# Kernel tuning notes

Hardware: AMD Instinct MI355X
Metric: run time of the kernel (lower is better)

Reference implementation:

```python
import jax, jax.numpy as jnp
import numpy as np

VOCAB = 32000
EMB = 512
HID = 1024
B = 64
LPRE = 256
MAXL = 16


def _gru(x, Wih, Whh, bih, bhh):
    # x: (B, T, E); torch GRU gate order r, z, n
    Bb, T, E = x.shape
    H = Whh.shape[1]
    xW = jnp.einsum('bte,ge->btg', x, Wih) + bih  # (B, T, 3H)
    def step(h, xt):
        gh = h @ Whh.T + bhh
        r = jax.nn.sigmoid(xt[:, :H] + gh[:, :H])
        z = jax.nn.sigmoid(xt[:, H:2 * H] + gh[:, H:2 * H])
        n = jnp.tanh(xt[:, 2 * H:] + r * gh[:, 2 * H:])
        h = (1.0 - z) * n + z * h
        return h, h
    h0 = jnp.zeros((Bb, H), x.dtype)
    hT, ys = jax.lax.scan(step, h0, jnp.swapaxes(xW, 0, 1))
    return jnp.swapaxes(ys, 0, 1), hT


def setup_inputs() -> dict:
    key = jax.random.key(0)
    ks = jax.random.split(key, 24)
    s = 0.02
    inp = {
        'pre_seq': jax.random.randint(ks[0], (B, LPRE), 0, VOCAB),
        'post_seq': jax.random.randint(ks[1], (B, LPRE), 0, VOCAB),
        'trg': jax.random.randint(ks[2], (B, MAXL), 0, 2),
        'emb': jax.random.normal(ks[3], (VOCAB, EMB), jnp.float32) * s,
        'Wih_pre': jax.random.normal(ks[4], (3 * HID, EMB), jnp.float32) * s,
        'Whh_pre': jax.random.normal(ks[5], (3 * HID, HID), jnp.float32) * s,
        'bih_pre': jnp.zeros((3 * HID,), jnp.float32),
        'bhh_pre': jnp.zeros((3 * HID,), jnp.float32),
        'Wih_post': jax.random.normal(ks[6], (3 * HID, EMB), jnp.float32) * s,
        'Whh_post': jax.random.normal(ks[7], (3 * HID, HID), jnp.float32) * s,
        'bih_post': jnp.zeros((3 * HID,), jnp.float32),
        'bhh_post': jnp.zeros((3 * HID,), jnp.float32),
        'fc_W': jax.random.normal(ks[8], (HID, 2 * HID), jnp.float32) * s,
        'fc_b': jnp.zeros((HID,), jnp.float32),
        'attn_W': jax.random.normal(ks[9], (HID, 2 * HID), jnp.float32) * s,
        'attn_b': jnp.zeros((HID,), jnp.float32),
        'v_W': jax.random.normal(ks[10], (1, HID), jnp.float32) * s,
        'fc1_W': jax.random.normal(ks[11], (HID, HID), jnp.float32) * s,
        'fc1_b': jnp.zeros((HID,), jnp.float32),
        'fc2_W': jax.random.normal(ks[12], (HID, 2 * HID), jnp.float32) * s,
        'fc2_b': jnp.zeros((HID,), jnp.float32),
        'fco_W': jax.random.normal(ks[13], (1, 2 * HID), jnp.float32) * s,
        'fco_b': jnp.zeros((1,), jnp.float32),
    }
    return inp


def reference(pre_seq, post_seq, trg, emb,
              Wih_pre, Whh_pre, bih_pre, bhh_pre,
              Wih_post, Whh_post, bih_post, bhh_post,
              fc_W, fc_b, attn_W, attn_b, v_W,
              fc1_W, fc1_b, fc2_W, fc2_b, fco_W, fco_b):
    bsz, len_pre = pre_seq.shape
    max_len = trg.shape[1]
    # Encoder (dropout = identity, eval mode)
    pre_e = emb[pre_seq]
    post_e = emb[post_seq]
    pre_out, pre_h = _gru(pre_e, Wih_pre, Whh_pre, bih_pre, bhh_pre)
    post_out, post_h = _gru(post_e, Wih_post, Whh_post, bih_post, bhh_post)
    enc_out = jnp.concatenate([pre_out, post_out], axis=1)  # (B, 2*Lp, H)
    hidden = jnp.tanh(jnp.concatenate([pre_h, post_h], axis=-1) @ fc_W.T + fc_b)  # (B, H)
    # Decoder: hidden is never updated in the original loop, so one step suffices;
    # the per-t result is identical and is broadcast over max_len.
    src_len = enc_out.shape[1]
    hid_rep = jnp.broadcast_to(hidden[:, None, :], (bsz, src_len, hidden.shape[-1]))
    energy = jnp.tanh(jnp.concatenate([hid_rep, enc_out], axis=-1) @ attn_W.T + attn_b)
    a = jax.nn.softmax(jnp.einsum('bsh,h->bs', energy, v_W[0]), axis=1)  # (B, S)
    weighted = jnp.einsum('bs,bsh->bh', a, enc_out)  # (B, H)
    o = jnp.tanh(hidden @ fc1_W.T + fc1_b)
    o = jnp.tanh(jnp.concatenate([o, weighted], axis=1) @ fc2_W.T + fc2_b)  # (B, H)
    o_rep = jnp.broadcast_to(o[:, None, :], (bsz, src_len, o.shape[-1]))
    feat = jax.nn.relu(jnp.concatenate([enc_out, o_rep], axis=-1))  # (B, S, 2H)
    logits = jnp.einsum('bsf,of->bso', feat, fco_W) + fco_b  # (B, S, 1)
    sig = jax.nn.sigmoid(logits)
    outputs_pre = jnp.broadcast_to(sig[:, None, :len_pre, :], (bsz, max_len, len_pre, 1))
    outputs_post = jnp.broadcast_to(sig[:, None, len_pre:, :], (bsz, max_len, len_pre, 1))
    return outputs_pre, outputs_post
```

## Files before the change

### kernel.cpp

```cpp
#include <hip/hip_runtime.h>
#include <math.h>

#define BATCH 64
#define LPRE 256
#define EMBD 512
#define HID 1024
#define G3 3072
#define SRC 512
#define VOCAB 32000

typedef unsigned int uint32;
typedef unsigned long long u64;
typedef short bf16x8 __attribute__((ext_vector_type(8)));
typedef float f32x4 __attribute__((ext_vector_type(4)));
typedef uint32 u32x4 __attribute__((ext_vector_type(4)));

__device__ __forceinline__ float frcp_(float x) { return __builtin_amdgcn_rcpf(x); }
__device__ __forceinline__ float sigmoidf_(float x) {
    x = fminf(fmaxf(x, -30.f), 30.f);
    return frcp_(1.0f + __expf(-x));
}
__device__ __forceinline__ float tanhf_(float x) {
    x = fminf(fmaxf(x, -15.f), 15.f);
    float e = __expf(2.f * x);
    return (e - 1.f) * frcp_(e + 1.f);
}

__device__ __forceinline__ unsigned short f2bf(float f) {
    uint32 u = __float_as_uint(f);
    return (unsigned short)((u + 0x7fffu + ((u >> 16) & 1u)) >> 16);
}
__device__ __forceinline__ float bf2f(unsigned short s) { return __uint_as_float(((uint32)s) << 16); }
__device__ __forceinline__ uint4 pack8(float4 a, float4 b) {
    uint4 w;
    w.x = (uint32)f2bf(a.x) | ((uint32)f2bf(a.y) << 16);
    w.y = (uint32)f2bf(a.z) | ((uint32)f2bf(a.w) << 16);
    w.z = (uint32)f2bf(b.x) | ((uint32)f2bf(b.y) << 16);
    w.w = (uint32)f2bf(b.z) | ((uint32)f2bf(b.w) << 16);
    return w;
}
__device__ __forceinline__ void up2(uint32 u, float& f0, float& f1) {
    f0 = __uint_as_float(u << 16);
    f1 = __uint_as_float(u & 0xffff0000u);
}

struct CvtSeg { const float* src; unsigned short* dst; int ld, off, colshift; uint32 gend; };
struct CvtArgs { CvtSeg s[10]; uint32 total; };

__global__ __launch_bounds__(256) void kcvtN(CvtArgs a) {
    uint32 stride = gridDim.x * 256;
    for (uint32 g = blockIdx.x * 256 + threadIdx.x; g < a.total; g += stride) {
        uint32 gs = 0;
#pragma unroll
        for (int k = 0; k < 10; k++) {
            if (g < a.s[k].gend) {
                uint32 lg = g - gs;
                size_t e = (size_t)lg * 4;
                int r = (int)(e >> a.s[k].colshift);
                int c = (int)(e & (((size_t)1 << a.s[k].colshift) - 1));
                const float* sp = a.s[k].src + (size_t)r * a.s[k].ld + a.s[k].off + c;
                float4 v = *(const float4*)sp;
                uint2 w;
                w.x = (uint32)f2bf(v.x) | ((uint32)f2bf(v.y) << 16);
                w.y = (uint32)f2bf(v.z) | ((uint32)f2bf(v.w) << 16);
                *(uint2*)(a.s[k].dst + e) = w;
                break;
            }
            gs = a.s[k].gend;
        }
    }
}

__global__ __launch_bounds__(256) void kproj(const int* __restrict__ pre_seq,
                                             const int* __restrict__ post_seq, int t0,
                                             const float* __restrict__ emb,
                                             const unsigned short* __restrict__ embb,
                                             const unsigned short* __restrict__ Wihb,
                                             const float* __restrict__ bih_pre,
                                             const float* __restrict__ bih_post,
                                             unsigned short* __restrict__ xw, int chunk) {
    __shared__ uint4 Asl[4][128];
    __shared__ uint4 Bsl[4][128];
    __shared__ int tok[128];
    int gru = blockIdx.z;
    const int* seq = gru ? post_seq : pre_seq;
    const unsigned short* Wb = Wihb + (size_t)gru * G3 * EMBD;
    const float* bih = gru ? bih_post : bih_pre;
    unsigned short* xwout = xw + (size_t)gru * BATCH * chunk * G3;
    int tid = threadIdx.x;
    int row0 = blockIdx.x * 128, col0 = blockIdx.y * 128;
    if (tid < 128) {
        int rr = row0 + tid;
        tok[tid] = seq[(rr / chunk) * LPRE + t0 + (rr % chunk)];
    }
    __syncthreads();
    int lane = tid & 63, w = tid >> 6;
    int wm = w >> 1, wn = w & 1;
    int q = lane >> 4, m = lane & 15;
    int r0s = tid & 127, g0s = tid >> 7;
    int g1s = g0s + 2;
    f32x4 acc[4][4] = {};
    for (int kk = 0; kk < EMBD; kk += 32) {
        uint4 apack0, apack1;
        if (embb) {
            apack0 = *(const uint4*)(embb + (size_t)tok[r0s] * EMBD + kk + g0s * 8);
            apack1 = *(const uint4*)(embb + (size_t)tok[r0s] * EMBD + kk + g1s * 8);
        } else {
            const float* a0p = emb + (size_t)tok[r0s] * EMBD + kk + g0s * 8;
            const float* a1p = emb + (size_t)tok[r0s] * EMBD + kk + g1s * 8;
            float4 av00 = *(const float4*)a0p, av01 = *(const float4*)(a0p + 4);
            float4 av10 = *(const float4*)a1p, av11 = *(const float4*)(a1p + 4);
            apack0 = pack8(av00, av01);
            apack1 = pack8(av10, av11);
        }
        uint4 bv0 = *(const uint4*)(Wb + (size_t)(col0 + r0s) * EMBD + kk + g0s * 8);
        uint4 bv1 = *(const uint4*)(Wb + (size_t)(col0 + r0s) * EMBD + kk + g1s * 8);
        __syncthreads();
        Asl[g0s][r0s ^ (g0s << 2)] = apack0;
        Asl[g1s][r0s ^ (g1s << 2)] = apack1;
        Bsl[g0s][r0s ^ (g0s << 2)] = bv0;
        Bsl[g1s][r0s ^ (g1s << 2)] = bv1;
        __syncthreads();
        bf16x8 af[4], bfv[4];
#pragma unroll
        for (int i = 0; i < 4; i++) af[i] = *(bf16x8*)&Asl[q][(wm * 64 + i * 16 + m) ^ (q << 2)];
#pragma unroll
        for (int j = 0; j < 4; j++) bfv[j] = *(bf16x8*)&Bsl[q][(wn * 64 + j * 16 + m) ^ (q << 2)];
#pragma unroll
        for (int i = 0; i < 4; i++)
#pragma unroll
            for (int j = 0; j < 4; j++)
                acc[i][j] = __builtin_amdgcn_mfma_f32_16x16x32_bf16(af[i], bfv[j], acc[i][j], 0, 0, 0);
    }
#pragma unroll
    for (int i = 0; i < 4; i++)
#pragma unroll
        for (int j = 0; j < 4; j++)
#pragma unroll
            for (int reg = 0; reg < 4; reg++) {
                int row = row0 + wm * 64 + i * 16 + q * 4 + reg;
                int col = col0 + wn * 64 + j * 16 + m;
                xwout[(size_t)row * G3 + col] = f2bf(acc[i][j][reg] + bih[col]);
            }
}

__global__ __launch_bounds__(512, 2) void kstepP(unsigned short* __restrict__ hbp,
                                                 float* __restrict__ hf,
                                                 const unsigned short* __restrict__ Whhb,
                                                 const float* __restrict__ bhh0,
                                                 const float* __restrict__ bhh1,
                                                 const unsigned short* __restrict__ xw,
                                                 unsigned short* __restrict__ enc,
                                                 uint32* __restrict__ bar,
                                                 int t0, int chunk) {
    __shared__ float gl[8][32][3][17];
    __shared__ unsigned short hsh[32][16];
    int gru = blockIdx.z;
    int mh = blockIdx.y;
    int u0 = blockIdx.x * 16;
    int tid = threadIdx.x;
    int ks = tid >> 6;
    int lane = tid & 63;
    int q = lane >> 4, m = lane & 15;
    int bbase = mh * 32;
    const unsigned short* Wg = Whhb + (size_t)gru * G3 * HID;
    const float* bhh = gru ? bhh1 : bhh0;

    int dom = gru * 2 + mh;
    uint32* slots = bar + (size_t)dom * 128;
    uint32* gen = bar + 512 + (size_t)dom * 32;
    int sid = blockIdx.x;
    bool leader = (blockIdx.x == 0);

    bf16x8 bfrag[3][4];
#pragma unroll
    for (int g = 0; g < 3; ++g) {
        const unsigned short* pb = Wg + (size_t)(g * HID + u0 + m) * HID + ks * 128 + q * 8;
#pragma unroll
        for (int it = 0; it < 4; ++it) bfrag[g][it] = *(const bf16x8*)(pb + it * 32);
    }
#pragma unroll
    for (int g = 0; g < 3; ++g)
#pragma unroll
        for (int it = 0; it < 4; ++it) asm volatile("" : "+v"(bfrag[g][it]));

    int bl = tid >> 4, ul = tid & 15;
    int be = bbase + bl, ue = u0 + ul;
    float brr = bhh[ue], bzz = bhh[HID + ue], bnn = bhh[2 * HID + ue];
    unsigned short h16r = __hip_atomic_load(
        &hbp[(size_t)(((t0 & 1) * 2 + gru) * BATCH + be) * HID + ue],
        __ATOMIC_RELAXED, __HIP_MEMORY_SCOPE_AGENT);

    const unsigned short* xwb = xw + ((size_t)(gru * BATCH + be) * chunk) * G3;
    float xr = bf2f(xwb[ue]);
    float xz = bf2f(xwb[HID + ue]);
    float xn = bf2f(xwb[2 * HID + ue]);

    for (int tl = 0; tl < chunk; ++tl) {
        int t = t0 + tl;
        int p = t & 1;
        const unsigned short* hb = hbp + ((size_t)p * 2 + gru) * BATCH * HID;
        unsigned short* hob = hbp + ((size_t)(p ^ 1) * 2 + gru) * BATCH * HID;

        const unsigned short* pa0 = hb + (size_t)(bbase + m) * HID + ks * 128 + q * 8;
        const unsigned short* pa1 = pa0 + (size_t)16 * HID;
        u32x4 av0[4], av1[4];
#pragma unroll
        for (int it = 0; it < 4; ++it) {
            asm volatile("global_load_dwordx4 %0, %1, off sc0 sc1"
                         : "=v"(av0[it]) : "v"(pa0 + it * 32));
            asm volatile("global_load_dwordx4 %0, %1, off sc0 sc1"
                         : "=v"(av1[it]) : "v"(pa1 + it * 32));
        }
        asm volatile("s_waitcnt vmcnt(0)" ::: "memory");
        __builtin_amdgcn_sched_barrier(0);

        f32x4 acc[3][2] = {};
#pragma unroll
        for (int it = 0; it < 4; ++it)
#pragma unroll
            for (int g = 0; g < 3; ++g) {
                acc[g][0] = __builtin_amdgcn_mfma_f32_16x16x32_bf16(*(bf16x8*)&av0[it], bfrag[g][it], acc[g][0], 0, 0, 0);
                acc[g][1] = __builtin_amdgcn_mfma_f32_16x16x32_bf16(*(bf16x8*)&av1[it], bfrag[g][it], acc[g][1], 0, 0, 0);
            }
#pragma unroll
        for (int g = 0; g < 3; ++g)
#pragma unroll
            for (int reg = 0; reg < 4; ++reg) {
                gl[ks][q * 4 + reg][g][m] = acc[g][0][reg];
                gl[ks][16 + q * 4 + reg][g][m] = acc[g][1][reg];
            }
        __syncthreads();
        float ar = 0.f, az = 0.f, an = 0.f;
#pragma unroll
        for (int k2 = 0; k2 < 8; ++k2) {
            ar += gl[k2][bl][0][ul];
            az += gl[k2][bl][1][ul];
            an += gl[k2][bl][2][ul];
        }
        float r = sigmoidf_(xr + ar + brr);
        float z = sigmoidf_(xz + az + bzz);
        float n = tanhf_(xn + r * (an + bnn));
        float hnew = (1.f - z) * n + z * bf2f(h16r);
        unsigned short h16 = f2bf(hnew);
        h16r = h16;
        hsh[bl][ul] = h16;
        enc[((size_t)be * SRC + gru * LPRE + t) * HID + ue] = h16;
        if (t == LPRE - 1) hf[((size_t)gru * BATCH + be) * HID + ue] = hnew;
        __syncthreads();
        if (tid < 64) {
            int row = tid >> 1, half = tid & 1;
            u32x4 hv = *(const u32x4*)&hsh[row][half * 8];
            unsigned short* dst = hob + (size_t)(bbase + row) * HID + u0 + half * 8;
            asm volatile("global_store_dwordx4 %0, %1, off sc0 sc1"
                         :: "v"(dst), "v"(hv) : "memory");
        }
        if (tl < chunk - 1) {
            uint32 t1 = (uint32)(t + 1);
            if (tid < 64)
                asm volatile("s_waitcnt vmcnt(0)" ::: "memory");
            if (tid == 0)
                __hip_atomic_store(&slots[sid], t1, __ATOMIC_RELAXED, __HIP_MEMORY_SCOPE_AGENT);
            const unsigned short* xwn = xwb + (size_t)(tl + 1) * G3;
            xr = bf2f(xwn[ue]);
            xz = bf2f(xwn[HID + ue]);
            xn = bf2f(xwn[2 * HID + ue]);
            if (leader && tid < 64) {
                for (;;) {
                    uint32 s0 = __hip_atomic_load(&slots[tid], __ATOMIC_RELAXED, __HIP_MEMORY_SCOPE_AGENT);
                    if (__all(s0 >= t1)) break;
                    __builtin_amdgcn_s_sleep(1);
                }
                if (tid == 0)
                    __hip_atomic_store(gen, t1, __ATOMIC_RELAXED, __HIP_MEMORY_SCOPE_AGENT);
            }
            if (tid == 0) {
                while (__hip_atomic_load(gen, __ATOMIC_RELAXED, __HIP_MEMORY_SCOPE_AGENT) < t1)
                    __builtin_amdgcn_s_sleep(1);
            }
            __syncthreads();
        }
    }
}

__global__ __launch_bounds__(256) void kg64(const float* __restrict__ A1, int K1,
                                            const float* __restrict__ A2, int K2,
                                            const unsigned short* __restrict__ Wb,
                                            const float* __restrict__ bias,
                                            float* __restrict__ out, int N, int act) {
    __shared__ uint4 Asl[4][64];
    int tid = threadIdx.x;
    int col0 = blockIdx.x * 64;
    int lane = tid & 63, w = tid >> 6;
    int q = lane >> 4, m = lane & 15;
    int K = K1 + K2;
    int arow = tid >> 2, akg = tid & 3;
    const unsigned short* wp = Wb + (size_t)(col0 + w * 16 + m) * K + q * 8;
    f32x4 acc[4] = {};
    for (int kk = 0; kk < K; kk += 32) {
        int k0 = kk + akg * 8;
        const float* ap = (k0 < K1) ? (A1 + (size_t)arow * K1 + k0)
                                    : (A2 + (size_t)arow * K2 + (k0 - K1));
        float4 v0 = *(const float4*)ap;
        float4 v1 = *(const float4*)(ap + 4);
        __syncthreads();
        Asl[akg][arow ^ (akg << 2)] = pack8(v0, v1);
        __syncthreads();
        bf16x8 bfv = *(const bf16x8*)(wp + kk);
        bf16x8 af[4];
#pragma unroll
        for (int i = 0; i < 4; i++) af[i] = *(bf16x8*)&Asl[q][(i * 16 + m) ^ (q << 2)];
#pragma unroll
        for (int i = 0; i < 4; i++)
            acc[i] = __builtin_amdgcn_mfma_f32_16x16x32_bf16(af[i], bfv, acc[i], 0, 0, 0);
    }
    int j = col0 + w * 16 + m;
    float bv = bias ? bias[j] : 0.f;
#pragma unroll
    for (int i = 0; i < 4; i++)
#pragma unroll
        for (int reg = 0; reg < 4; reg++) {
            int b = i * 16 + q * 4 + reg;
            float v = acc[i][reg] + bv;
            if (act == 1) v = tanhf_(v);
            out[(size_t)b * N + j] = v;
        }
}

__global__ __launch_bounds__(256) void kattn(const unsigned short* __restrict__ enc,
                                             const unsigned short* __restrict__ Wb,
                                             const float* __restrict__ attn_b,
                                             const float* __restrict__ hidA,
                                             const float* __restrict__ vW,
                                             const float* __restrict__ fcoW,
                                             float* __restrict__ e,
                                             float* __restrict__ dvec) {
    __shared__ uint4 Asl[4][128];
    __shared__ uint4 Bsl[4][128];
    __shared__ float red[2][128][17];
    __shared__ float dred[128][2];
    __shared__ float fsh[HID];
    int tid = threadIdx.x;
    int row0 = blockIdx.x * 128, col0 = blockIdx.y * 128;
    bool dwork = (blockIdx.y == 0);
    if (dwork)
        for (int l = tid; l < HID; l += 256) fsh[l] = fcoW[l];
    int lane = tid & 63, w = tid >> 6;
    int wm = w >> 1, wn = w & 1;
    int q = lane >> 4, m = lane & 15;
    int r0s = tid & 127, g0s = tid >> 7;
    int g1s = g0s + 2;
    f32x4 acc[4][4] = {};
    float dacc = 0.f;
    for (int kk = 0; kk < HID; kk += 32) {
        uint4 av0 = *(const uint4*)(enc + (size_t)(row0 + r0s) * HID + kk + g0s * 8);
        uint4 av1 = *(const uint4*)(enc + (size_t)(row0 + r0s) * HID + kk + g1s * 8);
        uint4 bv0 = *(const uint4*)(Wb + (size_t)(col0 + r0s) * HID + kk + g0s * 8);
        uint4 bv1 = *(const uint4*)(Wb + (size_t)(col0 + r0s) * HID + kk + g1s * 8);
        __syncthreads();
        Asl[g0s][r0s ^ (g0s << 2)] = av0;
        Asl[g1s][r0s ^ (g1s << 2)] = av1;
        Bsl[g0s][r0s ^ (g0s << 2)] = bv0;
        Bsl[g1s][r0s ^ (g1s << 2)] = bv1;
        __syncthreads();
        bf16x8 af[4], bfv[4];
#pragma unroll
        for (int i = 0; i < 4; i++) af[i] = *(bf16x8*)&Asl[q][(wm * 64 + i * 16 + m) ^ (q << 2)];
#pragma unroll
        for (int j = 0; j < 4; j++) bfv[j] = *(bf16x8*)&Bsl[q][(wn * 64 + j * 16 + m) ^ (q << 2)];
        if (dwork) {
            int r2 = tid >> 1, sp = tid & 1;
#pragma unroll
            for (int sg = 0; sg < 2; sg++) {
                int seg = sp * 2 + sg;
                uint4 v = Asl[seg][r2 ^ (seg << 2)];
                const uint32* vw = (const uint32*)&v;
#pragma unroll
                for (int wd = 0; wd < 4; wd++) {
                    float e0, e1;
                    up2(vw[wd], e0, e1);
                    int kb = kk + seg * 8 + wd * 2;
                    dacc += fmaxf(e0, 0.f) * fsh[kb] + fmaxf(e1, 0.f) * fsh[kb + 1];
                }
            }
        }
#pragma unroll
        for (int i = 0; i < 4; i++)
#pragma unroll
            for (int j = 0; j < 4; j++)
                acc[i][j] = __builtin_amdgcn_mfma_f32_16x16x32_bf16(af[i], bfv[j], acc[i][j], 0, 0, 0);
    }
    int b = row0 / SRC;
#pragma unroll
    for (int i = 0; i < 4; i++)
#pragma unroll
        for (int reg = 0; reg < 4; reg++) {
            int row_local = wm * 64 + i * 16 + q * 4 + reg;
            float s = 0.f;
#pragma unroll
            for (int j = 0; j < 4; j++) {
                int col = col0 + wn * 64 + j * 16 + m;
                float v = acc[i][j][reg] + hidA[(size_t)b * HID + col] + attn_b[col];
                s += vW[col] * tanhf(v);
            }
            red[wn][row_local][m] = s;
        }
    if (dwork) dred[tid >> 1][tid & 1] = dacc;
    __syncthreads();
    if (tid < 128) {
        float s = 0.f;
        for (int c = 0; c < 16; c++) s += red[0][tid][c] + red[1][tid][c];
        atomicAdd(e + row0 + tid, s);
        if (dwork) dvec[row0 + tid] = dred[tid][0] + dred[tid][1];
    }
}

__global__ __launch_bounds__(256) void kswW(const float* __restrict__ evec,
                                            const unsigned short* __restrict__ enc,
                                            float* __restrict__ wout) {
    __shared__ float red[256];
    __shared__ float asw[512];
    int b = blockIdx.y;
    int tid = threadIdx.x;
    float v0 = evec[(size_t)b * SRC + tid], v1 = evec[(size_t)b * SRC + 256 + tid];
    red[tid] = fmaxf(v0, v1);
    __syncthreads();
    for (int st = 128; st > 0; st >>= 1) {
        if (tid < st) red[tid] = fmaxf(red[tid], red[tid + st]);
        __syncthreads();
    }
    float mx = red[0];
    __syncthreads();
    float e0 = __expf(v0 - mx), e1 = __expf(v1 - mx);
    red[tid] = e0 + e1;
    __syncthreads();
    for (int st = 128; st > 0; st >>= 1) {
        if (tid < st) red[tid] += red[tid + st];
        __syncthreads();
    }
    float inv = 1.0f / red[0];
    asw[tid] = e0 * inv;
    asw[tid + 256] = e1 * inv;
    __syncthreads();
    int h = blockIdx.x * 256 + tid;
    float acc = 0.f;
    for (int s = 0; s < SRC; s++) acc += asw[s] * bf2f(enc[((size_t)b * SRC + s) * HID + h]);
    wout[(size_t)b * HID + h] = acc;
}

__global__ __launch_bounds__(256) void koc(const float* __restrict__ o2,
                                           const float* __restrict__ fcoW,
                                           float* __restrict__ oc) {
    int b = blockIdx.x;
    int tid = threadIdx.x;
    __shared__ float red[256];
    float s = 0.f;
    for (int j = tid; j < HID; j += 256) s += fmaxf(o2[(size_t)b * HID + j], 0.f) * fcoW[HID + j];
    red[tid] = s;
    __syncthreads();
    for (int st = 128; st > 0; st >>= 1) {
        if (tid < st) red[tid] += red[tid + st];
        __syncthreads();
    }
    if (tid == 0) oc[b] = red[0];
}

__global__ __launch_bounds__(256) void kout(const float* __restrict__ dvec,
                                            const float* __restrict__ oc,
                                            const float* __restrict__ fcob,
                                            float* __restrict__ out) {
    int idx = blockIdx.x * 256 + threadIdx.x;
    int b = idx >> 9, s = idx & 511;
    float logit = dvec[idx] + oc[b] + fcob[0];
    float sig = frcp_(1.f + __expf(-fminf(fmaxf(logit, -30.f), 30.f)));
    size_t base = (s < LPRE) ? ((size_t)b * 4096 + s)
                             : (262144 + (size_t)b * 4096 + (s - 256));
    for (int l = 0; l < 16; l++) out[base + (size_t)l * 256] = sig;
}

extern "C" void kernel_launch(void* const* d_in, const int* in_sizes, int n_in,
                              void* d_out, int out_size, void* d_ws, size_t ws_size,
                              hipStream_t stream) {
    (void)in_sizes; (void)n_in; (void)out_size;
    const int* pre_seq = (const int*)d_in[0];
    const int* post_seq = (const int*)d_in[1];
    const float* emb = (const float*)d_in[3];
    const float* Wih_pre = (const float*)d_in[4];
    const float* Whh_pre = (const float*)d_in[5];
    const float* bih_pre = (const float*)d_in[6];
    const float* bhh_pre = (const float*)d_in[7];
    const float* Wih_post = (const float*)d_in[8];
    const float* Whh_post = (const float*)d_in[9];
    const float* bih_post = (const float*)d_in[10];
    const float* bhh_post = (const float*)d_in[11];
    const float* fc_W = (const float*)d_in[12];
    const float* fc_b = (const float*)d_in[13];
    const float* attn_W = (const float*)d_in[14];
    const float* attn_b = (const float*)d_in[15];
    const float* v_W = (const float*)d_in[16];
    const float* fc1_W = (const float*)d_in[17];
    const float* fc1_b = (const float*)d_in[18];
    const float* fc2_W = (const float*)d_in[19];
    const float* fc2_b = (const float*)d_in[20];
    const float* fco_W = (const float*)d_in[21];
    const float* fco_b = (const float*)d_in[22];
    float* out = (float*)d_out;

    const size_t fixed_bytes = 103420160ull + 65536;
    int CH = (ws_size >= fixed_bytes + (size_t)2 * BATCH * 64 * G3 * 2) ? 64 : 32;

    char* ws = (char*)d_ws;
    unsigned short* xw = (unsigned short*)ws;     ws += (size_t)2 * BATCH * CH * G3 * 2;
    unsigned short* enc = (unsigned short*)ws;    ws += (size_t)BATCH * SRC * HID * 2;
    unsigned short* hbp = (unsigned short*)ws;    ws += (size_t)2 * 2 * BATCH * HID * 2;
    float* hf = (float*)ws;                       ws += (size_t)2 * BATCH * HID * 4;
    unsigned short* Wihb = (unsigned short*)ws;   ws += (size_t)2 * G3 * EMBD * 2;
    unsigned short* Whhb = (unsigned short*)ws;   ws += (size_t)2 * G3 * HID * 2;
    unsigned short* attnWb = (unsigned short*)ws; ws += (size_t)HID * HID * 2;
    unsigned short* attnWa = (unsigned short*)ws; ws += (size_t)HID * HID * 2;
    unsigned short* fcWb = (unsigned short*)ws;   ws += (size_t)HID * 2 * HID * 2;
    unsigned short* fc1b = (unsigned short*)ws;   ws += (size_t)HID * HID * 2;
    unsigned short* fc2b = (unsigned short*)ws;   ws += (size_t)HID * 2 * HID * 2;
    uint32* bar = (uint32*)ws;                    ws += 4096;
    float* dvec = (float*)ws;                     ws += (size_t)BATCH * SRC * 4;
    float* hidden = (float*)ws;                   ws += (size_t)BATCH * HID * 4;
    float* hidA = (float*)ws;                     ws += (size_t)BATCH * HID * 4;
    float* evec = (float*)ws;                     ws += (size_t)BATCH * SRC * 4;
    float* avec = (float*)ws;                     ws += (size_t)BATCH * SRC * 4;
    float* wsum = (float*)ws;                     ws += (size_t)BATCH * HID * 4;
    float* o1 = (float*)ws;                       ws += (size_t)BATCH * HID * 4;
    float* o2 = (float*)ws;                       ws += (size_t)BATCH * HID * 4;
    float* oc = (float*)ws;                       ws += (size_t)BATCH * 4;
    (void)avec;
    size_t emb_bytes = (size_t)VOCAB * EMBD * 2;
    unsigned short* embb = (unsigned short*)ws;
    int use_embb = ((size_t)((char*)(ws + 0) + emb_bytes - (char*)d_ws) <= ws_size) ? 1 : 0;

    hipMemsetAsync(hbp, 0, (size_t)2 * 2 * BATCH * HID * 2, stream);
    hipMemsetAsync(evec, 0, (size_t)BATCH * SRC * 4, stream);
    hipMemsetAsync(bar, 0, 4096, stream);

    {
        CvtArgs a;
        uint32 cum = 0;
        int k = 0;
        auto add = [&](const float* src, unsigned short* dst, int ld, int off, int colshift, uint32 ngrp) {
            cum += ngrp;
            a.s[k].src = src; a.s[k].dst = dst; a.s[k].ld = ld; a.s[k].off = off;
            a.s[k].colshift = colshift; a.s[k].gend = cum; k++;
        };
        if (use_embb) add(emb, embb, EMBD, 0, 9, (uint32)(VOCAB * EMBD / 4));
        add(Wih_pre, Wihb, EMBD, 0, 9, G3 * EMBD / 4);
        add(Wih_post, Wihb + (size_t)G3 * EMBD, EMBD, 0, 9, G3 * EMBD / 4);
        add(Whh_pre, Whhb, HID, 0, 10, G3 * HID / 4);
        add(Whh_post, Whhb + (size_t)G3 * HID, HID, 0, 10, G3 * HID / 4);
        add(attn_W, attnWb, 2 * HID, HID, 10, HID * HID / 4);
        add(attn_W, attnWa, 2 * HID, 0, 10, HID * HID / 4);
        add(fc1_W, fc1b, HID, 0, 10, HID * HID / 4);
        add(fc_W, fcWb, 2 * HID, 0, 11, HID * 2 * HID / 4);
        add(fc2_W, fc2b, 2 * HID, 0, 11, HID * 2 * HID / 4);
        while (k < 10) {
            a.s[k].src = Wih_pre; a.s[k].dst = Wihb; a.s[k].ld = EMBD; a.s[k].off = 0;
            a.s[k].colshift = 9; a.s[k].gend = cum; k++;
        }
        a.total = cum;
        kcvtN<<<2048, 256, 0, stream>>>(a);
    }

    const unsigned short* embb_arg = use_embb ? embb : (const unsigned short*)nullptr;
    for (int c = 0; c < LPRE / CH; c++) {
        kproj<<<dim3(BATCH * CH / 128, G3 / 128, 2), 256, 0, stream>>>(
            pre_seq, post_seq, c * CH, emb, embb_arg, Wihb, bih_pre, bih_post, xw, CH);
        kstepP<<<dim3(64, 2, 2), 512, 0, stream>>>(hbp, hf, Whhb, bhh_pre, bhh_post,
                                                   xw, enc, bar, c * CH, CH);
    }
    float* pre_h = hf;
    float* post_h = hf + (size_t)BATCH * HID;

    kg64<<<HID / 64, 256, 0, stream>>>(pre_h, HID, post_h, HID, fcWb, fc_b, hidden, HID, 1);
    kg64<<<HID / 64, 256, 0, stream>>>(hidden, HID, (const float*)nullptr, 0, attnWa,
                                       (const float*)nullptr, hidA, HID, 0);
    kattn<<<dim3(BATCH * SRC / 128, HID / 128), 256, 0, stream>>>(enc, attnWb, attn_b, hidA,
                                                                  v_W, fco_W, evec, dvec);
    kswW<<<dim3(HID / 256, BATCH), 256, 0, stream>>>(evec, enc, wsum);
    kg64<<<HID / 64, 256, 0, stream>>>(hidden, HID, (const float*)nullptr, 0, fc1b, fc1_b, o1, HID, 1);
    kg64<<<HID / 64, 256, 0, stream>>>(o1, HID, wsum, HID, fc2b, fc2_b, o2, HID, 1);
    koc<<<BATCH, 256, 0, stream>>>(o2, fco_W, oc);
    kout<<<BATCH * SRC / 256, 256, 0, stream>>>(dvec, oc, fco_b, out);
}
```

Measured before the change: 1.872 ms.

## Fuse GRU input projection into the persistent recurrent step kernel

Removes the separate kproj GEMM and its per-chunk launches. The persistent kstepP kernel now keeps the Wih fragments in registers and computes the next timestep's x·Wih + bih with MFMA while the current step finishes. The result is double-buffered in shared memory. This avoids the xw round-trip through global memory and the chunked relaunches. The cost is extra registers, extra MFMA and syncthreads work inside the latency-critical recurrent loop, and mandatory use of the bf16 embedding copy.

```diff
diff --git a/kernel.cpp b/kernel.cpp
--- a/kernel.cpp
+++ b/kernel.cpp
@@ -71,90 +71,22 @@
     }
 }
 
-__global__ __launch_bounds__(256) void kproj(const int* __restrict__ pre_seq,
-                                             const int* __restrict__ post_seq, int t0,
-                                             const float* __restrict__ emb,
-                                             const unsigned short* __restrict__ embb,
-                                             const unsigned short* __restrict__ Wihb,
-                                             const float* __restrict__ bih_pre,
-                                             const float* __restrict__ bih_post,
-                                             unsigned short* __restrict__ xw, int chunk) {
-    __shared__ uint4 Asl[4][128];
-    __shared__ uint4 Bsl[4][128];
-    __shared__ int tok[128];
-    int gru = blockIdx.z;
-    const int* seq = gru ? post_seq : pre_seq;
-    const unsigned short* Wb = Wihb + (size_t)gru * G3 * EMBD;
-    const float* bih = gru ? bih_post : bih_pre;
-    unsigned short* xwout = xw + (size_t)gru * BATCH * chunk * G3;
-    int tid = threadIdx.x;
-    int row0 = blockIdx.x * 128, col0 = blockIdx.y * 128;
-    if (tid < 128) {
-        int rr = row0 + tid;
-        tok[tid] = seq[(rr / chunk) * LPRE + t0 + (rr % chunk)];
-    }
-    __syncthreads();
-    int lane = tid & 63, w = tid >> 6;
-    int wm = w >> 1, wn = w & 1;
-    int q = lane >> 4, m = lane & 15;
-    int r0s = tid & 127, g0s = tid >> 7;
-    int g1s = g0s + 2;
-    f32x4 acc[4][4] = {};
-    for (int kk = 0; kk < EMBD; kk += 32) {
-        uint4 apack0, apack1;
-        if (embb) {
-            apack0 = *(const uint4*)(embb + (size_t)tok[r0s] * EMBD + kk + g0s * 8);
-            apack1 = *(const uint4*)(embb + (size_t)tok[r0s] * EMBD + kk + g1s * 8);
-        } else {
-            const float* a0p = emb + (size_t)tok[r0s] * EMBD + kk + g0s * 8;
-            const float* a1p = emb + (size_t)tok[r0s] * EMBD + kk + g1s * 8;
-            float4 av00 = *(const float4*)a0p, av01 = *(const float4*)(a0p + 4);
-            float4 av10 = *(const float4*)a1p, av11 = *(const float4*)(a1p + 4);
-            apack0 = pack8(av00, av01);
-            apack1 = pack8(av10, av11);
-        }
-        uint4 bv0 = *(const uint4*)(Wb + (size_t)(col0 + r0s) * EMBD + kk + g0s * 8);
-        uint4 bv1 = *(const uint4*)(Wb + (size_t)(col0 + r0s) * EMBD + kk + g1s * 8);
-        __syncthreads();
-        Asl[g0s][r0s ^ (g0s << 2)] = apack0;
-        Asl[g1s][r0s ^ (g1s << 2)] = apack1;
-        Bsl[g0s][r0s ^ (g0s << 2)] = bv0;
-        Bsl[g1s][r0s ^ (g1s << 2)] = bv1;
-        __syncthreads();
-        bf16x8 af[4], bfv[4];
-#pragma unroll
-        for (int i = 0; i < 4; i++) af[i] = *(bf16x8*)&Asl[q][(wm * 64 + i * 16 + m) ^ (q << 2)];
-#pragma unroll
-        for (int j = 0; j < 4; j++) bfv[j] = *(bf16x8*)&Bsl[q][(wn * 64 + j * 16 + m) ^ (q << 2)];
-#pragma unroll
-        for (int i = 0; i < 4; i++)
-#pragma unroll
-            for (int j = 0; j < 4; j++)
-                acc[i][j] = __builtin_amdgcn_mfma_f32_16x16x32_bf16(af[i], bfv[j], acc[i][j], 0, 0, 0);
-    }
-#pragma unroll
-    for (int i = 0; i < 4; i++)
-#pragma unroll
-        for (int j = 0; j < 4; j++)
-#pragma unroll
-            for (int reg = 0; reg < 4; reg++) {
-                int row = row0 + wm * 64 + i * 16 + q * 4 + reg;
-                int col = col0 + wn * 64 + j * 16 + m;
-                xwout[(size_t)row * G3 + col] = f2bf(acc[i][j][reg] + bih[col]);
-            }
-}
-
 __global__ __launch_bounds__(512, 2) void kstepP(unsigned short* __restrict__ hbp,
                                                  float* __restrict__ hf,
                                                  const unsigned short* __restrict__ Whhb,
+                                                 const unsigned short* __restrict__ Wihb,
+                                                 const unsigned short* __restrict__ embb,
+                                                 const int* __restrict__ pre_seq,
+                                                 const int* __restrict__ post_seq,
                                                  const float* __restrict__ bhh0,
                                                  const float* __restrict__ bhh1,
-                                                 const unsigned short* __restrict__ xw,
+                                                 const float* __restrict__ bih0,
+                                                 const float* __restrict__ bih1,
                                                  unsigned short* __restrict__ enc,
-                                                 uint32* __restrict__ bar,
-                                                 int t0, int chunk) {
+                                                 uint32* __restrict__ bar) {
     __shared__ float gl[8][32][3][17];
     __shared__ unsigned short hsh[32][16];
+    __shared__ unsigned short xsh[2][32][3][16];
     int gru = blockIdx.z;
     int mh = blockIdx.y;
     int u0 = blockIdx.x * 16;
@@ -164,7 +96,10 @@
     int q = lane >> 4, m = lane & 15;
     int bbase = mh * 32;
     const unsigned short* Wg = Whhb + (size_t)gru * G3 * HID;
+    const unsigned short* Wx = Wihb + (size_t)gru * G3 * EMBD;
+    const int* seq = gru ? post_seq : pre_seq;
     const float* bhh = gru ? bhh1 : bhh0;
+    const float* bih = gru ? bih1 : bih0;
 
     int dom = gru * 2 + mh;
     uint32* slots = bar + (size_t)dom * 128;
@@ -179,28 +114,72 @@
 #pragma unroll
         for (int it = 0; it < 4; ++it) bfrag[g][it] = *(const bf16x8*)(pb + it * 32);
     }
-#pragma unroll
-    for (int g = 0; g < 3; ++g)
+    bf16x8 bx[3][2];
+#pragma unroll
+    for (int g = 0; g < 3; ++g) {
+        const unsigned short* pb = Wx + (size_t)(g * HID + u0 + m) * EMBD + ks * 64 + q * 8;
+#pragma unroll
+        for (int it = 0; it < 2; ++it) bx[g][it] = *(const bf16x8*)(pb + it * 32);
+    }
+#pragma unroll
+    for (int g = 0; g < 3; ++g) {
 #pragma unroll
         for (int it = 0; it < 4; ++it) asm volatile("" : "+v"(bfrag[g][it]));
+#pragma unroll
+        for (int it = 0; it < 2; ++it) asm volatile("" : "+v"(bx[g][it]));
+    }
 
     int bl = tid >> 4, ul = tid & 15;
     int be = bbase + bl, ue = u0 + ul;
     float brr = bhh[ue], bzz = bhh[HID + ue], bnn = bhh[2 * HID + ue];
+    float bihr = bih[ue], bihz = bih[HID + ue], bihn = bih[2 * HID + ue];
     unsigned short h16r = __hip_atomic_load(
-        &hbp[(size_t)(((t0 & 1) * 2 + gru) * BATCH + be) * HID + ue],
+        &hbp[(size_t)(gru)*BATCH * HID + (size_t)be * HID + ue],
         __ATOMIC_RELAXED, __HIP_MEMORY_SCOPE_AGENT);
 
-    const unsigned short* xwb = xw + ((size_t)(gru * BATCH + be) * chunk) * G3;
-    float xr = bf2f(xwb[ue]);
-    float xz = bf2f(xwb[HID + ue]);
-    float xn = bf2f(xwb[2 * HID + ue]);
-
-    for (int tl = 0; tl < chunk; ++tl) {
-        int t = t0 + tl;
-        int p = t & 1;
+    const int* seqr0 = seq + (size_t)(bbase + m) * LPRE;
+    const int* seqr1 = seq + (size_t)(bbase + 16 + m) * LPRE;
+
+    {
+        int ta = seqr0[0], tb = seqr1[0];
+        const unsigned short* ea = embb + (size_t)ta * EMBD + ks * 64 + q * 8;
+        const unsigned short* eb = embb + (size_t)tb * EMBD + ks * 64 + q * 8;
+        bf16x8 a00 = *(const bf16x8*)ea, a01 = *(const bf16x8*)(ea + 32);
+        bf16x8 a10 = *(const bf16x8*)eb, a11 = *(const bf16x8*)(eb + 32);
+        f32x4 ax[2][3] = {};
+#pragma unroll
+        for (int g = 0; g < 3; ++g) {
+            ax[0][g] = __builtin_amdgcn_mfma_f32_16x16x32_bf16(a00, bx[g][0], ax[0][g], 0, 0, 0);
+            ax[0][g] = __builtin_amdgcn_mfma_f32_16x16x32_bf16(a01, bx[g][1], ax[0][g], 0, 0, 0);
+            ax[1][g] = __builtin_amdgcn_mfma_f32_16x16x32_bf16(a10, bx[g][0], ax[1][g], 0, 0, 0);
+            ax[1][g] = __builtin_amdgcn_mfma_f32_16x16x32_bf16(a11, bx[g][1], ax[1][g], 0, 0, 0);
+        }
+#pragma unroll
+        for (int g = 0; g < 3; ++g)
+#pragma unroll
+            for (int reg = 0; reg < 4; ++reg) {
+                gl[ks][q * 4 + reg][g][m] = ax[0][g][reg];
+                gl[ks][16 + q * 4 + reg][g][m] = ax[1][g][reg];
+            }
+        __syncthreads();
+        float s0 = 0.f, s1 = 0.f, s2 = 0.f;
+#pragma unroll
+        for (int k2 = 0; k2 < 8; ++k2) {
+            s0 += gl[k2][bl][0][ul];
+            s1 += gl[k2][bl][1][ul];
+            s2 += gl[k2][bl][2][ul];
+        }
+        xsh[0][bl][0][ul] = f2bf(s0 + bihr);
+        xsh[0][bl][1][ul] = f2bf(s1 + bihz);
+        xsh[0][bl][2][ul] = f2bf(s2 + bihn);
+        __syncthreads();
+    }
+
+    for (int tl = 0; tl < LPRE; ++tl) {
+        int p = tl & 1;
         const unsigned short* hb = hbp + ((size_t)p * 2 + gru) * BATCH * HID;
         unsigned short* hob = hbp + ((size_t)(p ^ 1) * 2 + gru) * BATCH * HID;
+        bool more = (tl < LPRE - 1);
 
         const unsigned short* pa0 = hb + (size_t)(bbase + m) * HID + ks * 128 + q * 8;
         const unsigned short* pa1 = pa0 + (size_t)16 * HID;
@@ -230,6 +209,14 @@
                 gl[ks][q * 4 + reg][g][m] = acc[g][0][reg];
                 gl[ks][16 + q * 4 + reg][g][m] = acc[g][1][reg];
             }
+        bf16x8 a00, a01, a10, a11;
+        if (more) {
+            int ta = seqr0[tl + 1], tb = seqr1[tl + 1];
+            const unsigned short* ea = embb + (size_t)ta * EMBD + ks * 64 + q * 8;
+            const unsigned short* eb = embb + (size_t)tb * EMBD + ks * 64 + q * 8;
+            a00 = *(const bf16x8*)ea; a01 = *(const bf16x8*)(ea + 32);
+            a10 = *(const bf16x8*)eb; a11 = *(const bf16x8*)(eb + 32);
+        }
         __syncthreads();
         float ar = 0.f, az = 0.f, an = 0.f;
 #pragma unroll
@@ -238,6 +225,9 @@
             az += gl[k2][bl][1][ul];
             an += gl[k2][bl][2][ul];
         }
+        float xr = bf2f(xsh[p][bl][0][ul]);
+        float xz = bf2f(xsh[p][bl][1][ul]);
+        float xn = bf2f(xsh[p][bl][2][ul]);
         float r = sigmoidf_(xr + ar + brr);
         float z = sigmoidf_(xz + az + bzz);
         float n = tanhf_(xn + r * (an + bnn));
@@ -245,9 +235,28 @@
         unsigned short h16 = f2bf(hnew);
         h16r = h16;
         hsh[bl][ul] = h16;
-        enc[((size_t)be * SRC + gru * LPRE + t) * HID + ue] = h16;
-        if (t == LPRE - 1) hf[((size_t)gru * BATCH + be) * HID + ue] = hnew;
-        __syncthreads();
+        enc[((size_t)be * SRC + gru * LPRE + tl) * HID + ue] = h16;
+        if (tl == LPRE - 1) hf[((size_t)gru * BATCH + be) * HID + ue] = hnew;
+        f32x4 ax[2][3] = {};
+        if (more) {
+#pragma unroll
+            for (int g = 0; g < 3; ++g) {
+                ax[0][g] = __builtin_amdgcn_mfma_f32_16x16x32_bf16(a00, bx[g][0], ax[0][g], 0, 0, 0);
+                ax[0][g] = __builtin_amdgcn_mfma_f32_16x16x32_bf16(a01, bx[g][1], ax[0][g], 0, 0, 0);
+                ax[1][g] = __builtin_amdgcn_mfma_f32_16x16x32_bf16(a10, bx[g][0], ax[1][g], 0, 0, 0);
+                ax[1][g] = __builtin_amdgcn_mfma_f32_16x16x32_bf16(a11, bx[g][1], ax[1][g], 0, 0, 0);
+            }
+        }
+        __syncthreads();
+        if (more) {
+#pragma unroll
+            for (int g = 0; g < 3; ++g)
+#pragma unroll
+                for (int reg = 0; reg < 4; ++reg) {
+                    gl[ks][q * 4 + reg][g][m] = ax[0][g][reg];
+                    gl[ks][16 + q * 4 + reg][g][m] = ax[1][g][reg];
+                }
+        }
         if (tid < 64) {
             int row = tid >> 1, half = tid & 1;
             u32x4 hv = *(const u32x4*)&hsh[row][half * 8];
@@ -255,20 +264,27 @@
             asm volatile("global_store_dwordx4 %0, %1, off sc0 sc1"
                          :: "v"(dst), "v"(hv) : "memory");
         }
-        if (tl < chunk - 1) {
-            uint32 t1 = (uint32)(t + 1);
+        if (more) {
+            __syncthreads();
+            float s0 = 0.f, s1 = 0.f, s2 = 0.f;
+#pragma unroll
+            for (int k2 = 0; k2 < 8; ++k2) {
+                s0 += gl[k2][bl][0][ul];
+                s1 += gl[k2][bl][1][ul];
+                s2 += gl[k2][bl][2][ul];
+            }
+            xsh[p ^ 1][bl][0][ul] = f2bf(s0 + bihr);
+            xsh[p ^ 1][bl][1][ul] = f2bf(s1 + bihz);
+            xsh[p ^ 1][bl][2][ul] = f2bf(s2 + bihn);
+            uint32 t1 = (uint32)(tl + 1);
             if (tid < 64)
                 asm volatile("s_waitcnt vmcnt(0)" ::: "memory");
             if (tid == 0)
                 __hip_atomic_store(&slots[sid], t1, __ATOMIC_RELAXED, __HIP_MEMORY_SCOPE_AGENT);
-            const unsigned short* xwn = xwb + (size_t)(tl + 1) * G3;
-            xr = bf2f(xwn[ue]);
-            xz = bf2f(xwn[HID + ue]);
-            xn = bf2f(xwn[2 * HID + ue]);
             if (leader && tid < 64) {
                 for (;;) {
-                    uint32 s0 = __hip_atomic_load(&slots[tid], __ATOMIC_RELAXED, __HIP_MEMORY_SCOPE_AGENT);
-                    if (__all(s0 >= t1)) break;
+                    uint32 s = __hip_atomic_load(&slots[tid], __ATOMIC_RELAXED, __HIP_MEMORY_SCOPE_AGENT);
+                    if (__all(s >= t1)) break;
                     __builtin_amdgcn_s_sleep(1);
                 }
                 if (tid == 0)
@@ -481,7 +497,7 @@
 extern "C" void kernel_launch(void* const* d_in, const int* in_sizes, int n_in,
                               void* d_out, int out_size, void* d_ws, size_t ws_size,
                               hipStream_t stream) {
-    (void)in_sizes; (void)n_in; (void)out_size;
+    (void)in_sizes; (void)n_in; (void)out_size; (void)ws_size;
     const int* pre_seq = (const int*)d_in[0];
     const int* post_seq = (const int*)d_in[1];
     const float* emb = (const float*)d_in[3];
@@ -506,14 +522,11 @@
     const float* fco_b = (const float*)d_in[22];
     float* out = (float*)d_out;
 
-    const size_t fixed_bytes = 103420160ull + 65536;
-    int CH = (ws_size >= fixed_bytes + (size_t)2 * BATCH * 64 * G3 * 2) ? 64 : 32;
-
     char* ws = (char*)d_ws;
-    unsigned short* xw = (unsigned short*)ws;     ws += (size_t)2 * BATCH * CH * G3 * 2;
     unsigned short* enc = (unsigned short*)ws;    ws += (size_t)BATCH * SRC * HID * 2;
     unsigned short* hbp = (unsigned short*)ws;    ws += (size_t)2 * 2 * BATCH * HID * 2;
     float* hf = (float*)ws;                       ws += (size_t)2 * BATCH * HID * 4;
+    unsigned short* embb = (unsigned short*)ws;   ws += (size_t)VOCAB * EMBD * 2;
     unsigned short* Wihb = (unsigned short*)ws;   ws += (size_t)2 * G3 * EMBD * 2;
     unsigned short* Whhb = (unsigned short*)ws;   ws += (size_t)2 * G3 * HID * 2;
     unsigned short* attnWb = (unsigned short*)ws; ws += (size_t)HID * HID * 2;
@@ -526,15 +539,10 @@
     float* hidden = (float*)ws;                   ws += (size_t)BATCH * HID * 4;
     float* hidA = (float*)ws;                     ws += (size_t)BATCH * HID * 4;
     float* evec = (float*)ws;                     ws += (size_t)BATCH * SRC * 4;
-    float* avec = (float*)ws;                     ws += (size_t)BATCH * SRC * 4;
     float* wsum = (float*)ws;                     ws += (size_t)BATCH * HID * 4;
     float* o1 = (float*)ws;                       ws += (size_t)BATCH * HID * 4;
     float* o2 = (float*)ws;                       ws += (size_t)BATCH * HID * 4;
     float* oc = (float*)ws;                       ws += (size_t)BATCH * 4;
-    (void)avec;
-    size_t emb_bytes = (size_t)VOCAB * EMBD * 2;
-    unsigned short* embb = (unsigned short*)ws;
-    int use_embb = ((size_t)((char*)(ws + 0) + emb_bytes - (char*)d_ws) <= ws_size) ? 1 : 0;
 
     hipMemsetAsync(hbp, 0, (size_t)2 * 2 * BATCH * HID * 2, stream);
     hipMemsetAsync(evec, 0, (size_t)BATCH * SRC * 4, stream);
@@ -549,7 +557,7 @@
             a.s[k].src = src; a.s[k].dst = dst; a.s[k].ld = ld; a.s[k].off = off;
             a.s[k].colshift = colshift; a.s[k].gend = cum; k++;
         };
-        if (use_embb) add(emb, embb, EMBD, 0, 9, (uint32)(VOCAB * EMBD / 4));
+        add(emb, embb, EMBD, 0, 9, (uint32)(VOCAB * EMBD / 4));
         add(Wih_pre, Wihb, EMBD, 0, 9, G3 * EMBD / 4);
         add(Wih_post, Wihb + (size_t)G3 * EMBD, EMBD, 0, 9, G3 * EMBD / 4);
         add(Whh_pre, Whhb, HID, 0, 10, G3 * HID / 4);
@@ -559,21 +567,14 @@
         add(fc1_W, fc1b, HID, 0, 10, HID * HID / 4);
         add(fc_W, fcWb, 2 * HID, 0, 11, HID * 2 * HID / 4);
         add(fc2_W, fc2b, 2 * HID, 0, 11, HID * 2 * HID / 4);
-        while (k < 10) {
-            a.s[k].src = Wih_pre; a.s[k].dst = Wihb; a.s[k].ld = EMBD; a.s[k].off = 0;
-            a.s[k].colshift = 9; a.s[k].gend = cum; k++;
-        }
         a.total = cum;
         kcvtN<<<2048, 256, 0, stream>>>(a);
     }
 
-    const unsigned short* embb_arg = use_embb ? embb : (const unsigned short*)nullptr;
-    for (int c = 0; c < LPRE / CH; c++) {
-        kproj<<<dim3(BATCH * CH / 128, G3 / 128, 2), 256, 0, stream>>>(
-            pre_seq, post_seq, c * CH, emb, embb_arg, Wihb, bih_pre, bih_post, xw, CH);
-        kstepP<<<dim3(64, 2, 2), 512, 0, stream>>>(hbp, hf, Whhb, bhh_pre, bhh_post,
-                                                   xw, enc, bar, c * CH, CH);
-    }
+    kstepP<<<dim3(64, 2, 2), 512, 0, stream>>>(hbp, hf, Whhb, Wihb, embb,
+                                               pre_seq, post_seq,
+                                               bhh_pre, bhh_post, bih_pre, bih_post,
+                                               enc, bar);
     float* pre_h = hf;
     float* post_h = hf + (size_t)BATCH * HID;
 
```

Result: slower. 1.933 ms (+3.3%).
